# Performance work log

Hardware: AMD Instinct MI355X
Metric: run time of the kernel (lower is better)

Reference implementation:

```python
import jax, jax.numpy as jnp
import numpy as np

B, L, H = 32, 512, 1024
H2 = H // 2          # split half = 512
D_ATTN = 64
EPS = 1e-5


def setup_inputs() -> dict:
    key = jax.random.key(0)
    ks = jax.random.split(key, 6)
    x = jax.random.normal(ks[0], (B, L, H), dtype=jnp.float32)
    # LayerNorm params (default torch init: weight=1, bias=0)
    ln_gamma = jnp.ones((H2,), jnp.float32)
    ln_beta = jnp.zeros((H2,), jnp.float32)
    # Toeplitz params (module inits w_vector=0, bias=1; use small random w for nontrivial math)
    w_vector = jax.random.normal(ks[1], (2 * L - 1,), jnp.float32) * 0.02
    t_bias = jnp.ones((L,), jnp.float32)
    # TinyAttention: kqv Linear(H2 -> 3*d_attn), proj Linear(d_attn -> H2)
    kqv_w = jax.random.normal(ks[2], (H2, 3 * D_ATTN), jnp.float32) * 0.02
    kqv_b = jnp.zeros((3 * D_ATTN,), jnp.float32)
    proj_w = jax.random.normal(ks[3], (D_ATTN, H2), jnp.float32) * 0.02
    proj_b = jnp.zeros((H2,), jnp.float32)
    return {"x": x, "ln_gamma": ln_gamma, "ln_beta": ln_beta,
            "w_vector": w_vector, "t_bias": t_bias,
            "kqv_w": kqv_w, "kqv_b": kqv_b, "proj_w": proj_w, "proj_b": proj_b}


def _toeplitz(w_vector):
    # Faithful replication of get_toeplitz(): pad, tile, trim, reshape, crop.
    r = w_vector.shape[0] // 2            # = L - 1
    t = jnp.pad(w_vector, (0, L))         # length 3L - 1
    t = jnp.tile(t, L)[:-L]               # length L * (3L - 2)
    t = t.reshape(L, 3 * L - 2)
    return t[:, r:-r]                      # [L, L]


def _tiny_attention(v, kqv_w, kqv_b, proj_w, proj_b):
    kqv = v @ kqv_w + kqv_b                        # [B, L, 3*d_attn]
    k, q, val = jnp.split(kqv, 3, axis=-1)         # chunk order: key, query, value
    scale = 1.0 / jnp.sqrt(jnp.float32(q.shape[-1]))
    scores = jnp.einsum('bqd,bkd->bqk', q, k) * scale
    soft = jax.nn.softmax(scores, axis=-1)
    head = jnp.einsum('bqk,bkd->bqd', soft, val)   # [B, L, d_attn]
    return head @ proj_w + proj_b                  # [B, L, H2]


def reference(x, ln_gamma, ln_beta, w_vector, t_bias, kqv_w, kqv_b, proj_w, proj_b):
    u, v = jnp.split(x, 2, axis=-1)                # each [B, L, H2]
    head = _tiny_attention(v, kqv_w, kqv_b, proj_w, proj_b)
    # LayerNorm over last dim
    mu = jnp.mean(v, axis=-1, keepdims=True)
    var = jnp.mean(jnp.square(v - mu), axis=-1, keepdims=True)
    vn = (v - mu) * jax.lax.rsqrt(var + EPS) * ln_gamma + ln_beta
    # spatial (Toeplitz) mixing: permute -> [B, H2, L], matmul [L, L], bias
    w_t = _toeplitz(w_vector)
    vm = jnp.einsum('blc,lm->bmc', vn, w_t.T).transpose(0, 2, 1)  # keep faithful: vp @ w_t
    vm = jnp.einsum('bcl,lm->bcm', vn.transpose(0, 2, 1), w_t) + t_bias
    v_out = vm.transpose(0, 2, 1) + head           # [B, L, H2]
    return u * v_out
```

## Files before the change

### kernel.cpp

```cpp
#include <hip/hip_runtime.h>
#include <math.h>

#define NB 32
#define LL 512
#define HH 1024
#define H2 512
#define DA 64

typedef unsigned int u32;
typedef unsigned short u16;
typedef __bf16 bf16x8 __attribute__((ext_vector_type(8)));
typedef float f32x4 __attribute__((ext_vector_type(4)));

__device__ __forceinline__ u16 f2bu(float f) {
    u32 u = __builtin_bit_cast(u32, f);
    u = (u + 0x7fff + ((u >> 16) & 1)) >> 16;
    return (u16)u;
}

__device__ __forceinline__ void async_cp16(const void* g, void* l) {
    __builtin_amdgcn_global_load_lds(
        (const __attribute__((address_space(1))) u32*)g,
        (__attribute__((address_space(3))) u32*)l, 16, 0, 0);
}

__global__ __launch_bounds__(256, 2)
void ln_t_kernel(const float* __restrict__ x,
                 const float* __restrict__ gamma, const float* __restrict__ beta,
                 const float* __restrict__ wv, const float* __restrict__ kqvw,
                 const float* __restrict__ projw,
                 u16* __restrict__ vnT, u16* __restrict__ wt,
                 u16* __restrict__ kqvwT, u16* __restrict__ projwT) {
    __shared__ u16 T[64 * 68];
    int blk = blockIdx.x, t = threadIdx.x;
#pragma unroll
    for (int s = 0; s < 6; ++s) {
        int e = blk * 1536 + s * 256 + t;
        if (e < 262144) {
            int m = e >> 9, l = e & 511;
            wt[e] = f2bu(wv[511 + m - l]);
        } else if (e < 262144 + 98304) {
            int i = e - 262144;
            int n = i >> 9, k = i & 511;
            kqvwT[i] = f2bu(kqvw[(size_t)k * 192 + n]);
        } else {
            int i = e - 360448;
            int c = i >> 6, d = i & 63;
            projwT[i] = f2bu(projw[(size_t)d * 512 + c]);
        }
    }
    int b = blk >> 3, l0 = (blk & 7) * 64;
    int r = t >> 2, q = t & 3;
    const float* xr = x + ((size_t)(b * LL + l0 + r)) * HH + H2;
    float s1 = 0.0f, s2 = 0.0f;
#pragma unroll
    for (int i = 0; i < 32; ++i) {
        float4 v = *(const float4*)(xr + q * 128 + i * 4);
        s1 += v.x + v.y + v.z + v.w;
        s2 += v.x * v.x + v.y * v.y + v.z * v.z + v.w * v.w;
    }
    s1 += __shfl_xor(s1, 1); s2 += __shfl_xor(s2, 1);
    s1 += __shfl_xor(s1, 2); s2 += __shfl_xor(s2, 2);
    float mu = s1 * (1.0f / H2);
    float rstd = rsqrtf(s2 * (1.0f / H2) - mu * mu + 1e-5f);
    for (int ct = 0; ct < 8; ++ct) {
        int cb = (t & 3) * 16;
#pragma unroll
        for (int i = 0; i < 4; ++i) {
            float4 v = *(const float4*)(xr + ct * 64 + cb + i * 4);
            int c = cb + i * 4;
            T[(c + 0) * 68 + r] = f2bu((v.x - mu) * rstd * gamma[ct * 64 + c + 0] + beta[ct * 64 + c + 0]);
            T[(c + 1) * 68 + r] = f2bu((v.y - mu) * rstd * gamma[ct * 64 + c + 1] + beta[ct * 64 + c + 1]);
            T[(c + 2) * 68 + r] = f2bu((v.z - mu) * rstd * gamma[ct * 64 + c + 2] + beta[ct * 64 + c + 2]);
            T[(c + 3) * 68 + r] = f2bu((v.w - mu) * rstd * gamma[ct * 64 + c + 3] + beta[ct * 64 + c + 3]);
        }
        __syncthreads();
        int c = t >> 2, lo = (t & 3) * 16;
        u16* dst = vnT + ((size_t)(b * H2 + ct * 64 + c)) * LL + l0 + lo;
        const u16* src = T + c * 68 + lo;
        ((ushort4*)dst)[0] = ((const ushort4*)src)[0];
        ((ushort4*)dst)[1] = ((const ushort4*)src)[1];
        ((ushort4*)dst)[2] = ((const ushort4*)src)[2];
        ((ushort4*)dst)[3] = ((const ushort4*)src)[3];
        __syncthreads();
    }
}

__global__ __launch_bounds__(256, 2)
void kqv_kernel(const float* __restrict__ x, const u16* __restrict__ wT,
                const float* __restrict__ bias,
                u16* __restrict__ qb, u16* __restrict__ kb, u16* __restrict__ vT) {
    __shared__ u16 As[32 * 72];
    __shared__ u16 Bs[192 * 64];
    u16* Ts = As;
    int r0 = blockIdx.x * 32;
    int t = threadIdx.x, lane = t & 63, wid = t >> 6;
    int wm = (wid & 1) * 16, wn = (wid >> 1) * 96;
    int l15 = lane & 15, q16 = lane >> 4, q8 = q16 * 8, s7 = l15 & 7;
    f32x4 acc[6] = {};
    for (int k0 = 0; k0 < 512; k0 += 64) {
#pragma unroll
        for (int s = 0; s < 6; ++s) {
            int ci = t + s * 256;
            int grow = ci >> 3, gcol = ((ci & 7) ^ (grow & 7)) << 3;
            async_cp16(wT + (size_t)grow * 512 + k0 + gcol, Bs + ci * 8);
        }
#pragma unroll
        for (int s = 0; s < 2; ++s) {
            int ci = t + s * 256;
            int row = ci >> 4, c4 = (ci & 15) * 4;
            float4 v = *(const float4*)(x + (size_t)(r0 + row) * HH + H2 + k0 + c4);
            ushort4 p;
            p.x = f2bu(v.x); p.y = f2bu(v.y); p.z = f2bu(v.z); p.w = f2bu(v.w);
            *(ushort4*)(As + row * 72 + c4) = p;
        }
        __syncthreads();
#pragma unroll
        for (int kk = 0; kk < 2; ++kk) {
            int j0 = kk * 4 + q16;
            bf16x8 a = *(const bf16x8*)(As + (wm + l15) * 72 + kk * 32 + q8);
#pragma unroll
            for (int j = 0; j < 6; ++j) {
                int n = wn + j * 16 + l15;
                bf16x8 bb = *(const bf16x8*)(Bs + (n * 8 + (j0 ^ (n & 7))) * 8);
                acc[j] = __builtin_amdgcn_mfma_f32_16x16x32_bf16(a, bb, acc[j], 0, 0, 0);
            }
        }
        __syncthreads();
    }
    int bidx = blockIdx.x >> 4, l0loc = (blockIdx.x & 15) * 32;
    int rq = q16 * 4;
#pragma unroll
    for (int r = 0; r < 4; ++r) {
        int mloc = wm + rq + r;
        size_t mg = (size_t)(r0 + mloc);
#pragma unroll
        for (int j = 0; j < 6; ++j) {
            int n = wn + j * 16 + l15;
            u16 hv = f2bu(acc[j][r] + bias[n]);
            if (n < 64)       kb[mg * 64 + n] = hv;
            else if (n < 128) qb[mg * 64 + (n - 64)] = hv;
            else              Ts[(n - 128) * 36 + mloc] = hv;
        }
    }
    __syncthreads();
    int d = t >> 2, lo = (t & 3) * 8;
    u16* dst = vT + ((size_t)(bidx * 64 + d)) * 512 + l0loc + lo;
    const u16* src = Ts + d * 36 + lo;
    ((ushort4*)dst)[0] = ((const ushort4*)src)[0];
    ((ushort4*)dst)[1] = ((const ushort4*)src)[1];
}

#define VLD 136
__global__ __launch_bounds__(256, 4)
void attn_kernel(const u16* __restrict__ qb, const u16* __restrict__ kb,
                 const u16* __restrict__ vT, u16* __restrict__ head) {
    __shared__ u16 Ps[4 * 16 * VLD];
    __shared__ float Osh[4][16 * 65];
    __shared__ float Msh[4][16], Lsh[4][16];
    int b = blockIdx.y, q0 = blockIdx.x * 16;
    int t = threadIdx.x, lane = t & 63, w = t >> 6;
    int l15 = lane & 15, q16 = lane >> 4, q8 = q16 * 8;
    int kc = w * 128;
    const u16* qg = qb + (size_t)b * LL * DA;
    const u16* kg = kb + (size_t)b * LL * DA;
    const u16* vg = vT + (size_t)b * DA * LL;

    bf16x8 aq[2];
#pragma unroll
    for (int s = 0; s < 2; ++s)
        aq[s] = *(const bf16x8*)(qg + (size_t)(q0 + l15) * DA + s * 32 + q8);

    f32x4 sc[8] = {};
#pragma unroll
    for (int j = 0; j < 8; ++j) {
#pragma unroll
        for (int s = 0; s < 2; ++s) {
            bf16x8 bk = *(const bf16x8*)(kg + (size_t)(kc + j * 16 + l15) * DA + s * 32 + q8);
            sc[j] = __builtin_amdgcn_mfma_f32_16x16x32_bf16(aq[s], bk, sc[j], 0, 0, 0);
        }
    }
    float mx[4], sm[4];
#pragma unroll
    for (int j = 0; j < 8; ++j)
#pragma unroll
        for (int r = 0; r < 4; ++r) sc[j][r] *= 0.125f;
#pragma unroll
    for (int r = 0; r < 4; ++r) {
        float m0 = sc[0][r];
#pragma unroll
        for (int j = 1; j < 8; ++j) m0 = fmaxf(m0, sc[j][r]);
        m0 = fmaxf(m0, __shfl_xor(m0, 1));
        m0 = fmaxf(m0, __shfl_xor(m0, 2));
        m0 = fmaxf(m0, __shfl_xor(m0, 4));
        m0 = fmaxf(m0, __shfl_xor(m0, 8));
        mx[r] = m0;
    }
#pragma unroll
    for (int j = 0; j < 8; ++j)
#pragma unroll
        for (int r = 0; r < 4; ++r) sc[j][r] = __expf(sc[j][r] - mx[r]);
#pragma unroll
    for (int r = 0; r < 4; ++r) {
        float s0 = sc[0][r];
#pragma unroll
        for (int j = 1; j < 8; ++j) s0 += sc[j][r];
        s0 += __shfl_xor(s0, 1);
        s0 += __shfl_xor(s0, 2);
        s0 += __shfl_xor(s0, 4);
        s0 += __shfl_xor(s0, 8);
        sm[r] = s0;
    }
    u16* Pw = Ps + w * 16 * VLD;
#pragma unroll
    for (int j = 0; j < 8; ++j)
#pragma unroll
        for (int r = 0; r < 4; ++r)
            Pw[(q16 * 4 + r) * VLD + j * 16 + l15] = f2bu(sc[j][r]);
    f32x4 o[4] = {};
#pragma unroll
    for (int kt = 0; kt < 4; ++kt) {
        bf16x8 ap = *(const bf16x8*)(Pw + l15 * VLD + kt * 32 + q8);
#pragma unroll
        for (int j = 0; j < 4; ++j) {
            bf16x8 bv = *(const bf16x8*)(vg + (size_t)(j * 16 + l15) * LL + kc + kt * 32 + q8);
            o[j] = __builtin_amdgcn_mfma_f32_16x16x32_bf16(ap, bv, o[j], 0, 0, 0);
        }
    }
#pragma unroll
    for (int j = 0; j < 4; ++j)
#pragma unroll
        for (int r = 0; r < 4; ++r)
            Osh[w][(q16 * 4 + r) * 65 + j * 16 + l15] = o[j][r];
    if (l15 == 0) {
#pragma unroll
        for (int r = 0; r < 4; ++r) {
            Msh[w][q16 * 4 + r] = mx[r];
            Lsh[w][q16 * 4 + r] = sm[r];
        }
    }
    __syncthreads();
    int qq = t >> 4, dg = (t & 15) * 4;
    float m0 = Msh[0][qq], m1 = Msh[1][qq], m2 = Msh[2][qq], m3 = Msh[3][qq];
    float ms = fmaxf(fmaxf(m0, m1), fmaxf(m2, m3));
    float f0 = __expf(m0 - ms), f1 = __expf(m1 - ms), f2 = __expf(m2 - ms), f3 = __expf(m3 - ms);
    float lst = Lsh[0][qq] * f0 + Lsh[1][qq] * f1 + Lsh[2][qq] * f2 + Lsh[3][qq] * f3;
    float inv = 1.0f / lst;
    ushort4 res;
    u16* rp = (u16*)&res;
#pragma unroll
    for (int i = 0; i < 4; ++i) {
        int idx = qq * 65 + dg + i;
        float a = Osh[0][idx] * f0 + Osh[1][idx] * f1 + Osh[2][idx] * f2 + Osh[3][idx] * f3;
        rp[i] = f2bu(a * inv);
    }
    *(ushort4*)(head + (size_t)(b * LL + q0 + qq) * DA + dg) = res;
}

__device__ __forceinline__ void mfma_tile64(const u16* As, const u16* Bs,
                                            f32x4 acc[4][4], int wm, int wn,
                                            int l15, int q16) {
    int s7 = l15 & 7;
#pragma unroll
    for (int kk = 0; kk < 2; ++kk) {
        int j0 = kk * 4 + q16;
        bf16x8 a[4], bv[4];
#pragma unroll
        for (int i = 0; i < 4; ++i) {
            int row = wm + i * 16 + l15;
            a[i] = *(const bf16x8*)(As + (row * 8 + (j0 ^ s7)) * 8);
        }
#pragma unroll
        for (int j = 0; j < 4; ++j) {
            int row = wn + j * 16 + l15;
            bv[j] = *(const bf16x8*)(Bs + (row * 8 + (j0 ^ s7)) * 8);
        }
#pragma unroll
        for (int i = 0; i < 4; ++i)
#pragma unroll
            for (int j = 0; j < 4; ++j)
                acc[i][j] = __builtin_amdgcn_mfma_f32_16x16x32_bf16(a[i], bv[j], acc[i][j], 0, 0, 0);
    }
}

__global__ __launch_bounds__(256, 2)
void mix_kernel(const u16* __restrict__ wt,
                const u16* __restrict__ vnT,
                const u16* __restrict__ headb,
                const u16* __restrict__ projwT,
                const float* __restrict__ x,
                const float* __restrict__ tbias,
                const float* __restrict__ projb,
                float* __restrict__ out) {
    __shared__ u16 As[128 * 64];
    __shared__ u16 Bs[128 * 64];
    int b = blockIdx.z, m0 = blockIdx.y * 128, c0 = blockIdx.x * 128;
    int t = threadIdx.x, lane = t & 63, wid = t >> 6;
    int wm = (wid >> 1) * 64, wn = (wid & 1) * 64;
    int l15 = lane & 15, q16 = lane >> 4;
    f32x4 acc[4][4] = {};
    const u16* Ag = wt + (size_t)m0 * 512;
    const u16* Bg = vnT + ((size_t)b * H2 + c0) * 512;
    for (int k0 = 0; k0 < 512; k0 += 64) {
#pragma unroll
        for (int s = 0; s < 4; ++s) {
            int ci = t + s * 256;
            int grow = ci >> 3, gcol = ((ci & 7) ^ (grow & 7)) << 3;
            async_cp16(Ag + (size_t)grow * 512 + k0 + gcol, As + ci * 8);
            async_cp16(Bg + (size_t)grow * 512 + k0 + gcol, Bs + ci * 8);
        }
        __syncthreads();
        mfma_tile64(As, Bs, acc, wm, wn, l15, q16);
        __syncthreads();
    }
    {
        const u16* Hg = headb + ((size_t)b * LL + m0) * DA;
        const u16* Pg = projwT + (size_t)c0 * DA;
#pragma unroll
        for (int s = 0; s < 4; ++s) {
            int ci = t + s * 256;
            int grow = ci >> 3, gcol = ((ci & 7) ^ (grow & 7)) << 3;
            async_cp16(Hg + (size_t)grow * 64 + gcol, As + ci * 8);
            async_cp16(Pg + (size_t)grow * 64 + gcol, Bs + ci * 8);
        }
        __syncthreads();
        mfma_tile64(As, Bs, acc, wm, wn, l15, q16);
        __syncthreads();
    }
    int rq = q16 * 4;
#pragma unroll
    for (int i = 0; i < 4; ++i) {
#pragma unroll
        for (int r = 0; r < 4; ++r) {
            int m = m0 + wm + i * 16 + rq + r;
            float tb = tbias[m];
            const float* xrow = x + ((size_t)b * LL + m) * HH;
            float* orow = out + ((size_t)b * LL + m) * H2;
#pragma unroll
            for (int j = 0; j < 4; ++j) {
                int c = c0 + wn + j * 16 + l15;
                float val = acc[i][j][r] + tb + projb[c];
                orow[c] = xrow[c] * val;
            }
        }
    }
}

extern "C" void kernel_launch(void* const* d_in, const int* in_sizes, int n_in,
                              void* d_out, int out_size, void* d_ws, size_t ws_size,
                              hipStream_t stream) {
    (void)in_sizes; (void)n_in; (void)out_size; (void)ws_size;
    const float* x     = (const float*)d_in[0];
    const float* gamma = (const float*)d_in[1];
    const float* beta  = (const float*)d_in[2];
    const float* wv    = (const float*)d_in[3];
    const float* tb    = (const float*)d_in[4];
    const float* kqvw  = (const float*)d_in[5];
    const float* kqvb  = (const float*)d_in[6];
    const float* projw = (const float*)d_in[7];
    const float* projb = (const float*)d_in[8];
    float* out = (float*)d_out;

    u16* vnT_bf  = (u16*)d_ws;
    u16* qb      = vnT_bf + (size_t)NB * LL * H2;
    u16* kb      = qb + (size_t)NB * LL * DA;
    u16* vTb     = kb + (size_t)NB * LL * DA;
    u16* head_bf = vTb + (size_t)NB * LL * DA;
    u16* wt_bf   = head_bf + (size_t)NB * LL * DA;
    u16* kqvwT   = wt_bf + 512 * 512;
    u16* projwT  = kqvwT + 192 * 512;

    ln_t_kernel<<<256, 256, 0, stream>>>(x, gamma, beta, wv, kqvw, projw,
                                         vnT_bf, wt_bf, kqvwT, projwT);
    kqv_kernel <<<NB * LL / 32, 256, 0, stream>>>(x, kqvwT, kqvb, qb, kb, vTb);
    attn_kernel<<<dim3(32, NB), 256, 0, stream>>>(qb, kb, vTb, head_bf);
    mix_kernel <<<dim3(4, 4, NB), 256, 0, stream>>>(wt_bf, vnT_bf, head_bf, projwT,
                                                    x, tb, projb, out);
}
```

Baseline: 183.4 us.

## Fuse LayerNorm with KQV projection and remap mix kernel block order

The weight conversion moves into its own prep kernel, and the LayerNorm/transpose pass is fused with the KQV projection GEMM. Each block now handles 64 rows, so it reads the same x rows for both the norm and the projection, and one launch is dropped in favour of a small prep launch. The fused kernel doubles the MFMA tile per warp and reuses shared memory for the V transpose. The mix kernel uses a 1D grid with a remapped block order so that blocks running together are grouped by m-tile, aiming for better L2 reuse of the Toeplitz tile. The cost is fewer blocks in the fused stage (256), which may cut parallelism.

```diff
diff --git a/kernel.cpp b/kernel.cpp
--- a/kernel.cpp
+++ b/kernel.cpp
@@ -24,32 +24,41 @@
         (__attribute__((address_space(3))) u32*)l, 16, 0, 0);
 }
 
+__global__ void prep_kernel(const float* __restrict__ wv,
+                            const float* __restrict__ kqvw,
+                            const float* __restrict__ projw,
+                            u16* __restrict__ wt, u16* __restrict__ kqvwT,
+                            u16* __restrict__ projwT) {
+    int e = blockIdx.x * 256 + threadIdx.x;
+    if (e < 262144) {
+        int m = e >> 9, l = e & 511;
+        wt[e] = f2bu(wv[511 + m - l]);
+    } else if (e < 262144 + 98304) {
+        int i = e - 262144;
+        int n = i >> 9, k = i & 511;
+        kqvwT[i] = f2bu(kqvw[(size_t)k * 192 + n]);
+    } else {
+        int i = e - 360448;
+        int c = i >> 6, d = i & 63;
+        projwT[i] = f2bu(projw[(size_t)d * 512 + c]);
+    }
+}
+
 __global__ __launch_bounds__(256, 2)
-void ln_t_kernel(const float* __restrict__ x,
-                 const float* __restrict__ gamma, const float* __restrict__ beta,
-                 const float* __restrict__ wv, const float* __restrict__ kqvw,
-                 const float* __restrict__ projw,
-                 u16* __restrict__ vnT, u16* __restrict__ wt,
-                 u16* __restrict__ kqvwT, u16* __restrict__ projwT) {
-    __shared__ u16 T[64 * 68];
+void front_kernel(const float* __restrict__ x,
+                  const float* __restrict__ gamma, const float* __restrict__ beta,
+                  const u16* __restrict__ kqvwT, const float* __restrict__ kqvb,
+                  u16* __restrict__ vnT,
+                  u16* __restrict__ qb, u16* __restrict__ kb, u16* __restrict__ vT) {
+    __shared__ u16 smem[64 * 72 + 192 * 64];
+    u16* As = smem;
+    u16* Bs = smem + 64 * 72;
+    u16* T  = Bs;
     int blk = blockIdx.x, t = threadIdx.x;
-#pragma unroll
-    for (int s = 0; s < 6; ++s) {
-        int e = blk * 1536 + s * 256 + t;
-        if (e < 262144) {
-            int m = e >> 9, l = e & 511;
-            wt[e] = f2bu(wv[511 + m - l]);
-        } else if (e < 262144 + 98304) {
-            int i = e - 262144;
-            int n = i >> 9, k = i & 511;
-            kqvwT[i] = f2bu(kqvw[(size_t)k * 192 + n]);
-        } else {
-            int i = e - 360448;
-            int c = i >> 6, d = i & 63;
-            projwT[i] = f2bu(projw[(size_t)d * 512 + c]);
-        }
-    }
     int b = blk >> 3, l0 = (blk & 7) * 64;
+    int lane = t & 63, wid = t >> 6;
+    int l15 = lane & 15, q16 = lane >> 4, q8 = q16 * 8;
+
     int r = t >> 2, q = t & 3;
     const float* xr = x + ((size_t)(b * LL + l0 + r)) * HH + H2;
     float s1 = 0.0f, s2 = 0.0f;
@@ -63,6 +72,7 @@
     s1 += __shfl_xor(s1, 2); s2 += __shfl_xor(s2, 2);
     float mu = s1 * (1.0f / H2);
     float rstd = rsqrtf(s2 * (1.0f / H2) - mu * mu + 1e-5f);
+
     for (int ct = 0; ct < 8; ++ct) {
         int cb = (t & 3) * 16;
 #pragma unroll
@@ -84,32 +94,21 @@
         ((ushort4*)dst)[3] = ((const ushort4*)src)[3];
         __syncthreads();
     }
-}
-
-__global__ __launch_bounds__(256, 2)
-void kqv_kernel(const float* __restrict__ x, const u16* __restrict__ wT,
-                const float* __restrict__ bias,
-                u16* __restrict__ qb, u16* __restrict__ kb, u16* __restrict__ vT) {
-    __shared__ u16 As[32 * 72];
-    __shared__ u16 Bs[192 * 64];
-    u16* Ts = As;
-    int r0 = blockIdx.x * 32;
-    int t = threadIdx.x, lane = t & 63, wid = t >> 6;
-    int wm = (wid & 1) * 16, wn = (wid >> 1) * 96;
-    int l15 = lane & 15, q16 = lane >> 4, q8 = q16 * 8, s7 = l15 & 7;
-    f32x4 acc[6] = {};
+
+    int wm = (wid & 1) * 32, wn = (wid >> 1) * 96;
+    f32x4 acc[2][6] = {};
     for (int k0 = 0; k0 < 512; k0 += 64) {
 #pragma unroll
         for (int s = 0; s < 6; ++s) {
             int ci = t + s * 256;
             int grow = ci >> 3, gcol = ((ci & 7) ^ (grow & 7)) << 3;
-            async_cp16(wT + (size_t)grow * 512 + k0 + gcol, Bs + ci * 8);
-        }
-#pragma unroll
-        for (int s = 0; s < 2; ++s) {
+            async_cp16(kqvwT + (size_t)grow * 512 + k0 + gcol, Bs + ci * 8);
+        }
+#pragma unroll
+        for (int s = 0; s < 4; ++s) {
             int ci = t + s * 256;
             int row = ci >> 4, c4 = (ci & 15) * 4;
-            float4 v = *(const float4*)(x + (size_t)(r0 + row) * HH + H2 + k0 + c4);
+            float4 v = *(const float4*)(x + (size_t)(b * LL + l0 + row) * HH + H2 + k0 + c4);
             ushort4 p;
             p.x = f2bu(v.x); p.y = f2bu(v.y); p.z = f2bu(v.z); p.w = f2bu(v.w);
             *(ushort4*)(As + row * 72 + c4) = p;
@@ -118,37 +117,45 @@
 #pragma unroll
         for (int kk = 0; kk < 2; ++kk) {
             int j0 = kk * 4 + q16;
-            bf16x8 a = *(const bf16x8*)(As + (wm + l15) * 72 + kk * 32 + q8);
+            bf16x8 a[2];
+#pragma unroll
+            for (int i = 0; i < 2; ++i)
+                a[i] = *(const bf16x8*)(As + (wm + i * 16 + l15) * 72 + kk * 32 + q8);
 #pragma unroll
             for (int j = 0; j < 6; ++j) {
                 int n = wn + j * 16 + l15;
                 bf16x8 bb = *(const bf16x8*)(Bs + (n * 8 + (j0 ^ (n & 7))) * 8);
-                acc[j] = __builtin_amdgcn_mfma_f32_16x16x32_bf16(a, bb, acc[j], 0, 0, 0);
+#pragma unroll
+                for (int i = 0; i < 2; ++i)
+                    acc[i][j] = __builtin_amdgcn_mfma_f32_16x16x32_bf16(a[i], bb, acc[i][j], 0, 0, 0);
             }
         }
         __syncthreads();
     }
-    int bidx = blockIdx.x >> 4, l0loc = (blockIdx.x & 15) * 32;
+    u16* Ts = Bs;
     int rq = q16 * 4;
 #pragma unroll
-    for (int r = 0; r < 4; ++r) {
-        int mloc = wm + rq + r;
-        size_t mg = (size_t)(r0 + mloc);
-#pragma unroll
-        for (int j = 0; j < 6; ++j) {
-            int n = wn + j * 16 + l15;
-            u16 hv = f2bu(acc[j][r] + bias[n]);
-            if (n < 64)       kb[mg * 64 + n] = hv;
-            else if (n < 128) qb[mg * 64 + (n - 64)] = hv;
-            else              Ts[(n - 128) * 36 + mloc] = hv;
-        }
-    }
+    for (int i = 0; i < 2; ++i)
+#pragma unroll
+        for (int rr = 0; rr < 4; ++rr) {
+            int mloc = wm + i * 16 + rq + rr;
+            size_t mg = (size_t)(b * LL + l0 + mloc);
+#pragma unroll
+            for (int j = 0; j < 6; ++j) {
+                int n = wn + j * 16 + l15;
+                u16 hv = f2bu(acc[i][j][rr] + kqvb[n]);
+                if (n < 64)       kb[mg * 64 + n] = hv;
+                else if (n < 128) qb[mg * 64 + (n - 64)] = hv;
+                else              Ts[(n - 128) * 68 + mloc] = hv;
+            }
+        }
     __syncthreads();
-    int d = t >> 2, lo = (t & 3) * 8;
-    u16* dst = vT + ((size_t)(bidx * 64 + d)) * 512 + l0loc + lo;
-    const u16* src = Ts + d * 36 + lo;
-    ((ushort4*)dst)[0] = ((const ushort4*)src)[0];
-    ((ushort4*)dst)[1] = ((const ushort4*)src)[1];
+    int d = t >> 2, mo = (t & 3) * 16;
+    u16* dst = vT + ((size_t)(b * 64 + d)) * 512 + l0 + mo;
+    const u16* srcl = Ts + d * 68 + mo;
+#pragma unroll
+    for (int c = 0; c < 4; ++c)
+        ((ushort4*)dst)[c] = ((const ushort4*)srcl)[c];
 }
 
 #define VLD 136
@@ -184,39 +191,39 @@
 #pragma unroll
     for (int j = 0; j < 8; ++j)
 #pragma unroll
-        for (int r = 0; r < 4; ++r) sc[j][r] *= 0.125f;
-#pragma unroll
-    for (int r = 0; r < 4; ++r) {
-        float m0 = sc[0][r];
-#pragma unroll
-        for (int j = 1; j < 8; ++j) m0 = fmaxf(m0, sc[j][r]);
+        for (int rr = 0; rr < 4; ++rr) sc[j][rr] *= 0.125f;
+#pragma unroll
+    for (int rr = 0; rr < 4; ++rr) {
+        float m0 = sc[0][rr];
+#pragma unroll
+        for (int j = 1; j < 8; ++j) m0 = fmaxf(m0, sc[j][rr]);
         m0 = fmaxf(m0, __shfl_xor(m0, 1));
         m0 = fmaxf(m0, __shfl_xor(m0, 2));
         m0 = fmaxf(m0, __shfl_xor(m0, 4));
         m0 = fmaxf(m0, __shfl_xor(m0, 8));
-        mx[r] = m0;
+        mx[rr] = m0;
     }
 #pragma unroll
     for (int j = 0; j < 8; ++j)
 #pragma unroll
-        for (int r = 0; r < 4; ++r) sc[j][r] = __expf(sc[j][r] - mx[r]);
-#pragma unroll
-    for (int r = 0; r < 4; ++r) {
-        float s0 = sc[0][r];
-#pragma unroll
-        for (int j = 1; j < 8; ++j) s0 += sc[j][r];
+        for (int rr = 0; rr < 4; ++rr) sc[j][rr] = __expf(sc[j][rr] - mx[rr]);
+#pragma unroll
+    for (int rr = 0; rr < 4; ++rr) {
+        float s0 = sc[0][rr];
+#pragma unroll
+        for (int j = 1; j < 8; ++j) s0 += sc[j][rr];
         s0 += __shfl_xor(s0, 1);
         s0 += __shfl_xor(s0, 2);
         s0 += __shfl_xor(s0, 4);
         s0 += __shfl_xor(s0, 8);
-        sm[r] = s0;
+        sm[rr] = s0;
     }
     u16* Pw = Ps + w * 16 * VLD;
 #pragma unroll
     for (int j = 0; j < 8; ++j)
 #pragma unroll
-        for (int r = 0; r < 4; ++r)
-            Pw[(q16 * 4 + r) * VLD + j * 16 + l15] = f2bu(sc[j][r]);
+        for (int rr = 0; rr < 4; ++rr)
+            Pw[(q16 * 4 + rr) * VLD + j * 16 + l15] = f2bu(sc[j][rr]);
     f32x4 o[4] = {};
 #pragma unroll
     for (int kt = 0; kt < 4; ++kt) {
@@ -230,13 +237,13 @@
 #pragma unroll
     for (int j = 0; j < 4; ++j)
 #pragma unroll
-        for (int r = 0; r < 4; ++r)
-            Osh[w][(q16 * 4 + r) * 65 + j * 16 + l15] = o[j][r];
+        for (int rr = 0; rr < 4; ++rr)
+            Osh[w][(q16 * 4 + rr) * 65 + j * 16 + l15] = o[j][rr];
     if (l15 == 0) {
 #pragma unroll
-        for (int r = 0; r < 4; ++r) {
-            Msh[w][q16 * 4 + r] = mx[r];
-            Lsh[w][q16 * 4 + r] = sm[r];
+        for (int rr = 0; rr < 4; ++rr) {
+            Msh[w][q16 * 4 + rr] = mx[rr];
+            Lsh[w][q16 * 4 + rr] = sm[rr];
         }
     }
     __syncthreads();
@@ -294,7 +301,10 @@
                 float* __restrict__ out) {
     __shared__ u16 As[128 * 64];
     __shared__ u16 Bs[128 * 64];
-    int b = blockIdx.z, m0 = blockIdx.y * 128, c0 = blockIdx.x * 128;
+    int lid = blockIdx.x;
+    int p8 = lid & 7, rest = lid >> 3;
+    int mi = rest & 3, pair = (rest >> 2) * 8 + p8;
+    int b = pair >> 2, m0 = mi * 128, c0 = (pair & 3) * 128;
     int t = threadIdx.x, lane = t & 63, wid = t >> 6;
     int wm = (wid >> 1) * 64, wn = (wid & 1) * 64;
     int l15 = lane & 15, q16 = lane >> 4;
@@ -331,15 +341,15 @@
 #pragma unroll
     for (int i = 0; i < 4; ++i) {
 #pragma unroll
-        for (int r = 0; r < 4; ++r) {
-            int m = m0 + wm + i * 16 + rq + r;
+        for (int rr = 0; rr < 4; ++rr) {
+            int m = m0 + wm + i * 16 + rq + rr;
             float tb = tbias[m];
             const float* xrow = x + ((size_t)b * LL + m) * HH;
             float* orow = out + ((size_t)b * LL + m) * H2;
 #pragma unroll
             for (int j = 0; j < 4; ++j) {
                 int c = c0 + wn + j * 16 + l15;
-                float val = acc[i][j][r] + tb + projb[c];
+                float val = acc[i][j][rr] + tb + projb[c];
                 orow[c] = xrow[c] * val;
             }
         }
@@ -370,10 +380,10 @@
     u16* kqvwT   = wt_bf + 512 * 512;
     u16* projwT  = kqvwT + 192 * 512;
 
-    ln_t_kernel<<<256, 256, 0, stream>>>(x, gamma, beta, wv, kqvw, projw,
-                                         vnT_bf, wt_bf, kqvwT, projwT);
-    kqv_kernel <<<NB * LL / 32, 256, 0, stream>>>(x, kqvwT, kqvb, qb, kb, vTb);
-    attn_kernel<<<dim3(32, NB), 256, 0, stream>>>(qb, kb, vTb, head_bf);
-    mix_kernel <<<dim3(4, 4, NB), 256, 0, stream>>>(wt_bf, vnT_bf, head_bf, projwT,
-                                                    x, tb, projb, out);
-}
+    prep_kernel <<<1536, 256, 0, stream>>>(wv, kqvw, projw, wt_bf, kqvwT, projwT);
+    front_kernel<<<256, 256, 0, stream>>>(x, gamma, beta, kqvwT, kqvb,
+                                          vnT_bf, qb, kb, vTb);
+    attn_kernel <<<dim3(32, NB), 256, 0, stream>>>(qb, kb, vTb, head_bf);
+    mix_kernel  <<<512, 256, 0, stream>>>(wt_bf, vnT_bf, head_bf, projwT,
+                                          x, tb, projb, out);
+}
```

Result: no change. 181.4 us (-1.1%).
